# Optimization experiments

Hardware: AMD Instinct MI355X
Metric: run time of the kernel (lower is better)

The kernel has to match this reference:

```python
import jax, jax.numpy as jnp
import numpy as np

D_MODEL = 768
NHEAD = 12
HEAD_DIM = D_MODEL // NHEAD


def setup_inputs() -> dict:
    key = jax.random.key(0)
    ks = jax.random.split(key, 9)
    B, S = 1, 4096
    scale = 1.0 / np.sqrt(D_MODEL)
    x = jax.random.normal(ks[0], (B, S, D_MODEL), dtype=jnp.float32)
    # Linear params: weight [out,in] torch convention, bias [out]
    wq = jax.random.normal(ks[1], (D_MODEL, D_MODEL), dtype=jnp.float32) * scale
    bq = jnp.zeros((D_MODEL,), dtype=jnp.float32)
    wk = jax.random.normal(ks[2], (D_MODEL, D_MODEL), dtype=jnp.float32) * scale
    bk = jnp.zeros((D_MODEL,), dtype=jnp.float32)
    wv = jax.random.normal(ks[3], (D_MODEL, D_MODEL), dtype=jnp.float32) * scale
    bv = jnp.zeros((D_MODEL,), dtype=jnp.float32)
    wo = jax.random.normal(ks[4], (D_MODEL, D_MODEL), dtype=jnp.float32) * scale
    bo = jnp.zeros((D_MODEL,), dtype=jnp.float32)
    return {"x": x, "wq": wq, "bq": bq, "wk": wk, "bk": bk,
            "wv": wv, "bv": bv, "wo": wo, "bo": bo}


def reference(x, wq, bq, wk, bk, wv, bv, wo, bo):
    B, S, D = x.shape
    H, Hd = NHEAD, HEAD_DIM
    # projections (torch Linear: x @ W^T + b)
    q = (x @ wq.T + bq).reshape(B, S, H, Hd).transpose(0, 2, 1, 3)  # [B,H,S,Hd]
    k = (x @ wk.T + bk).reshape(B, S, H, Hd).transpose(0, 2, 1, 3)
    v = (x @ wv.T + bv).reshape(B, S, H, Hd).transpose(0, 2, 1, 3)
    scores = jnp.einsum('bhsd,bhtd->bhst', q, k) / jnp.sqrt(jnp.float32(Hd))  # [B,H,S,S]
    probs = jax.nn.softmax(scores, axis=-1)
    attn = jnp.einsum('bhst,bhtd->bhsd', probs, v)  # [B,H,S,Hd]
    attn = attn.transpose(0, 2, 1, 3).reshape(B, S, D)
    return attn @ wo.T + bo
```

## Files before the change

kernel.cpp:

```cpp
#include <hip/hip_runtime.h>
#include <hip/hip_bf16.h>

typedef __attribute__((ext_vector_type(8))) __bf16 bf16x8;
typedef __attribute__((ext_vector_type(4))) __bf16 bf16x4;
typedef __attribute__((ext_vector_type(4))) float f32x4;
typedef __attribute__((ext_vector_type(16))) float f32x16;
typedef __attribute__((ext_vector_type(2))) unsigned u32x2;

#define D_MODEL 768
#define SEQ     4096
#define NH      12
#define HD      64

#define QSCALE (0.125f * 1.44269504088896f)

__device__ __forceinline__ void gload_lds16(const void* g, void* l) {
    __builtin_amdgcn_global_load_lds(
        (const __attribute__((address_space(1))) void*)g,
        (__attribute__((address_space(3))) void*)l, 16, 0, 0);
}

__device__ __forceinline__ u32x2 plswap(unsigned a, unsigned b) {
    return __builtin_amdgcn_permlane32_swap(a, b, false, false);
}

__global__ __launch_bounds__(256) void cvt_kernel(
    const float* __restrict__ x,  const float* __restrict__ wq,
    const float* __restrict__ wk, const float* __restrict__ wv,
    const float* __restrict__ wo,
    __bf16* __restrict__ xb,  __bf16* __restrict__ wqb,
    __bf16* __restrict__ wkb, __bf16* __restrict__ wvb,
    __bf16* __restrict__ wob)
{
    const int XV = SEQ * D_MODEL / 4;
    const int WV = D_MODEL * D_MODEL / 4;
    const int total = XV + 4 * WV;
    for (int i = blockIdx.x * blockDim.x + threadIdx.x; i < total;
         i += gridDim.x * blockDim.x) {
        const float* src; __bf16* dst; int j;
        if      (i < XV)          { src = x;  dst = xb;  j = i; }
        else if (i < XV + WV)     { src = wq; dst = wqb; j = i - XV; }
        else if (i < XV + 2*WV)   { src = wk; dst = wkb; j = i - XV - WV; }
        else if (i < XV + 3*WV)   { src = wv; dst = wvb; j = i - XV - 2*WV; }
        else                      { src = wo; dst = wob; j = i - XV - 3*WV; }
        float4 v = ((const float4*)src)[j];
        bf16x4 o;
        o[0] = (__bf16)v.x; o[1] = (__bf16)v.y;
        o[2] = (__bf16)v.z; o[3] = (__bf16)v.w;
        ((bf16x4*)dst)[j] = o;
    }
}

__device__ __forceinline__ void gemm128_core(
    const __bf16* __restrict__ A, const __bf16* __restrict__ B, int KD,
    f32x4 acc[4][4], __bf16 (*As)[64], __bf16 (*Bs)[64])
{
    const int t = threadIdx.x;
    const int lane = t & 63, wid = t >> 6;
    const int wm = (wid & 1) * 64, wn = (wid >> 1) * 64;
    const int lr = lane & 15, lc = lane >> 4;
    const int rl = lane >> 3;
    const int cs = (lane & 7) ^ rl;

    const __bf16* ag = A + (size_t)(wid * 32 + rl) * KD + cs * 8;
    const __bf16* bg = B + (size_t)(wid * 32 + rl) * KD + cs * 8;

    for (int kt = 0; kt < KD / 64; ++kt) {
        __syncthreads();
        #pragma unroll
        for (int i = 0; i < 4; ++i) {
            gload_lds16(ag + (size_t)i * 8 * KD + kt * 64,
                        &As[wid * 32 + i * 8][0]);
            gload_lds16(bg + (size_t)i * 8 * KD + kt * 64,
                        &Bs[wid * 32 + i * 8][0]);
        }
        __syncthreads();

        #pragma unroll
        for (int kh = 0; kh < 2; ++kh) {
            bf16x8 af[4], bfr[4];
            #pragma unroll
            for (int mi = 0; mi < 4; ++mi)
                af[mi] = *(const bf16x8*)
                    &As[wm + mi * 16 + lr][(((kh << 2) | lc) ^ (lr & 7)) * 8];
            #pragma unroll
            for (int ni = 0; ni < 4; ++ni)
                bfr[ni] = *(const bf16x8*)
                    &Bs[wn + ni * 16 + lr][(((kh << 2) | lc) ^ (lr & 7)) * 8];
            __builtin_amdgcn_s_setprio(1);
            #pragma unroll
            for (int mi = 0; mi < 4; ++mi)
                #pragma unroll
                for (int ni = 0; ni < 4; ++ni)
                    acc[mi][ni] = __builtin_amdgcn_mfma_f32_16x16x32_bf16(
                        af[mi], bfr[ni], acc[mi][ni], 0, 0, 0);
            __builtin_amdgcn_s_setprio(0);
        }
    }
}

__global__ __launch_bounds__(256) void qkv_gemm(
    const __bf16* __restrict__ xb,
    const __bf16* __restrict__ wqb, const __bf16* __restrict__ wkb,
    const __bf16* __restrict__ wvb,
    const float* __restrict__ bq, const float* __restrict__ bk,
    const float* __restrict__ bv,
    __bf16* __restrict__ Qo, __bf16* __restrict__ Ko,
    __bf16* __restrict__ Vto)
{
    __shared__ __bf16 As[128][64];
    __shared__ __bf16 Bs[128][64];
    const int bm = blockIdx.x;
    const int seg = blockIdx.y / 6, bn = blockIdx.y % 6;
    const __bf16* B  = (seg == 0) ? wqb : (seg == 1) ? wkb : wvb;
    const float* bias = (seg == 0) ? bq : (seg == 1) ? bk : bv;

    f32x4 acc[4][4] = {};
    gemm128_core(xb + (size_t)bm * 128 * D_MODEL,
                 B  + (size_t)bn * 128 * D_MODEL, D_MODEL, acc, As, Bs);

    const int t = threadIdx.x, lane = t & 63, wid = t >> 6;
    const int wm = (wid & 1) * 64, wn = (wid >> 1) * 64;
    const int lr = lane & 15, lc = lane >> 4;
    const int m0 = bm * 128 + wm, n0 = bn * 128 + wn;

    if (seg < 2) {
        __bf16* O = (seg == 0) ? Qo : Ko;
        const float sc = (seg == 0) ? QSCALE : 1.0f;
        #pragma unroll
        for (int mi = 0; mi < 4; ++mi)
            #pragma unroll
            for (int ni = 0; ni < 4; ++ni) {
                int col = n0 + ni * 16 + lr;
                float bb = bias[col];
                #pragma unroll
                for (int r = 0; r < 4; ++r)
                    O[(size_t)(m0 + mi * 16 + lc * 4 + r) * D_MODEL + col] =
                        (__bf16)((acc[mi][ni][r] + bb) * sc);
            }
    } else {
        #pragma unroll
        for (int mi = 0; mi < 4; ++mi)
            #pragma unroll
            for (int ni = 0; ni < 4; ++ni) {
                int col = n0 + ni * 16 + lr;
                float bb = bias[col];
                bf16x4 pk;
                #pragma unroll
                for (int r = 0; r < 4; ++r)
                    pk[r] = (__bf16)(acc[mi][ni][r] + bb);
                *(bf16x4*)&Vto[(size_t)col * SEQ + m0 + mi * 16 + lc * 4] = pk;
            }
    }
}

__global__ __launch_bounds__(256) void attn_kernel(
    const __bf16* __restrict__ Q, const __bf16* __restrict__ K,
    const __bf16* __restrict__ Vt, __bf16* __restrict__ Attn)
{
    __shared__ __align__(16) char LDSc[49152];
    __bf16 (*Ks)[32][64] = (__bf16(*)[32][64])(LDSc);
    __bf16 (*Vs)[64][32] = (__bf16(*)[64][32])(LDSc + 24576);
    float* Mg = (float*)LDSc;
    float* Ml = (float*)(LDSc + 24576);

    const int bid = blockIdx.x;
    const int swz = (bid & 7) * 96 + (bid >> 3);
    const int h  = swz >> 6;
    const int q0 = (swz & 63) * 64;

    const int t = threadIdx.x, lane = t & 63, wid = t >> 6;
    const int qs = wid & 1, half = wid >> 1;
    const int ql = lane & 31, hi = lane >> 5;
    const int s7 = ql & 7;
    const int v2s = (ql >> 1) & 3;

    const int krl = lane >> 3, kcs = (lane & 7) ^ (lane >> 3);
    const int vrl = lane >> 2, vcs = (lane & 3) ^ ((lane >> 3) & 3);
    const __bf16* kg = K +
        (size_t)(half * 2048 + qs * 16 + krl) * D_MODEL + h * HD + kcs * 8;
    const __bf16* vg = Vt +
        (size_t)(h * HD + qs * 32 + vrl) * SEQ + half * 2048 + vcs * 8;

    const __bf16* qrow = Q + (size_t)(q0 + qs * 32 + ql) * D_MODEL + h * HD;
    bf16x8 qf[4];
    #pragma unroll
    for (int k4 = 0; k4 < 4; ++k4)
        qf[k4] = *(const bf16x8*)&qrow[k4 * 16 + hi * 8];

    f32x16 acc0 = {}, acc1 = {};
    f32x16 lacc = {};

    #define STAGE(BUF, TT) do {                                               \
        const __bf16* kgt = kg + (size_t)(TT) * 32 * D_MODEL;                 \
        const __bf16* vgt = vg + (TT) * 32;                                   \
        gload_lds16(kgt,                    &Ks[half*3 + (BUF)][qs*16][0]);   \
        gload_lds16(kgt + 8 * D_MODEL,      &Ks[half*3 + (BUF)][qs*16+8][0]); \
        gload_lds16(vgt,                    &Vs[half*3 + (BUF)][qs*32][0]);   \
        gload_lds16(vgt + (size_t)16 * SEQ, &Vs[half*3 + (BUF)][qs*32+16][0]);\
    } while (0)

    STAGE(0, 0);

    const int NT = 2048 / 32;

#define ATILE(CUR, NXT, PT, DOPF) do {                                        \
    if (DOPF) {                                                               \
        STAGE(NXT, PT);                                                       \
        asm volatile("s_waitcnt vmcnt(4)" ::: "memory");                      \
    } else {                                                                  \
        asm volatile("s_waitcnt vmcnt(0)" ::: "memory");                      \
    }                                                                         \
    __builtin_amdgcn_s_barrier();                                             \
    f32x16 st = {};                                                           \
    __builtin_amdgcn_s_setprio(1);                                            \
    _Pragma("unroll")                                                         \
    for (int k4 = 0; k4 < 4; ++k4) {                                          \
        bf16x8 kf = *(const bf16x8*)                                          \
            &Ks[half*3 + (CUR)][ql][((k4*2 + hi) ^ s7) * 8];                  \
        st = __builtin_amdgcn_mfma_f32_32x32x16_bf16(kf, qf[k4], st, 0,0,0);  \
    }                                                                         \
    __builtin_amdgcn_s_setprio(0);                                            \
                 \
    _Pragma("unroll")                                                         \
    for (int r = 0; r < 16; ++r) st[r] = exp2f(st[r]);                        \
    lacc += st;                                                               \
                                               \
    unsigned wA[4], wB[4];                                                    \
    _Pragma("unroll")                                                         \
    for (int g = 0; g < 4; ++g) {                                             \
        union { __bf16 h2[2]; unsigned u; } pa, pb;                           \
        pa.h2[0] = (__bf16)st[4*g + 0]; pa.h2[1] = (__bf16)st[4*g + 1];       \
        pb.h2[0] = (__bf16)st[4*g + 2]; pb.h2[1] = (__bf16)st[4*g + 3];       \
        wA[g] = pa.u; wB[g] = pb.u;                                           \
    }                                                                         \
    __builtin_amdgcn_s_setprio(1);                                            \
    _Pragma("unroll")                                                         \
    for (int kb = 0; kb < 2; ++kb) {                                          \
        u32x2 sA = plswap(wA[2*kb], wA[2*kb + 1]);                            \
        u32x2 sB = plswap(wB[2*kb], wB[2*kb + 1]);                            \
        union { unsigned u[4]; bf16x8 v; } fb;                                \
        fb.u[0] = sA[0]; fb.u[1] = sB[0]; fb.u[2] = sA[1]; fb.u[3] = sB[1];   \
        bf16x8 vf0 = *(const bf16x8*)                                         \
            &Vs[half*3 + (CUR)][ql][((kb*2 + hi) ^ v2s) * 8];                 \
        bf16x8 vf1 = *(const bf16x8*)                                         \
            &Vs[half*3 + (CUR)][32 + ql][((kb*2 + hi) ^ v2s) * 8];            \
        acc0 = __builtin_amdgcn_mfma_f32_32x32x16_bf16(vf0, fb.v, acc0,0,0,0);\
        acc1 = __builtin_amdgcn_mfma_f32_32x32x16_bf16(vf1, fb.v, acc1,0,0,0);\
    }                                                                         \
    __builtin_amdgcn_s_setprio(0);                                            \
} while (0)

    for (int kk = 0; kk < 63; kk += 3) {
        ATILE(0, 1, kk + 1, 1);
        ATILE(1, 2, kk + 2, 1);
        ATILE(2, 0, kk + 3, (kk + 3 < NT));
    }
    ATILE(0, 1, 0, 0);
#undef ATILE
#undef STAGE

    float l_r;
    {
        float t8[8];
        #pragma unroll
        for (int i = 0; i < 8; ++i) t8[i] = lacc[i] + lacc[i + 8];
        #pragma unroll
        for (int i = 0; i < 4; ++i) t8[i] += t8[i + 4];
        l_r = (t8[0] + t8[1]) + (t8[2] + t8[3]);
        u32x2 rp = plswap(__float_as_uint(l_r), __float_as_uint(l_r));
        l_r = __uint_as_float(rp[0]) + __uint_as_float(rp[1]);
    }

    __syncthreads();
    if (half == 1) {
        float* mybuf = Mg + qs * 2048 + lane * 32;
        #pragma unroll
        for (int j = 0; j < 4; ++j) {
            f32x4 v; v[0]=acc0[4*j]; v[1]=acc0[4*j+1]; v[2]=acc0[4*j+2]; v[3]=acc0[4*j+3];
            *(f32x4*)&mybuf[(j ^ s7) * 4] = v;
        }
        #pragma unroll
        for (int j = 0; j < 4; ++j) {
            f32x4 v; v[0]=acc1[4*j]; v[1]=acc1[4*j+1]; v[2]=acc1[4*j+2]; v[3]=acc1[4*j+3];
            *(f32x4*)&mybuf[((4 + j) ^ s7) * 4] = v;
        }
        Ml[qs * 64 + lane] = l_r;
    }
    __syncthreads();
    if (half == 0) {
        float l1 = Ml[qs * 64 + lane];
        float li = 1.0f / (l_r + l1);
        const float* obuf = Mg + qs * 2048 + lane * 32;

        __bf16* orow = Attn + (size_t)(q0 + qs * 32 + ql) * D_MODEL
                       + h * HD + hi * 4;
        #pragma unroll
        for (int g = 0; g < 4; ++g) {
            f32x4 a1 = *(const f32x4*)&obuf[(g ^ s7) * 4];
            union { __bf16 h4[4]; uint2 v2; } w;
            #pragma unroll
            for (int i = 0; i < 4; ++i)
                w.h4[i] = (__bf16)((acc0[4*g+i] + a1[i]) * li);
            *(uint2*)&orow[g * 8] = w.v2;

            f32x4 b1 = *(const f32x4*)&obuf[((4 + g) ^ s7) * 4];
            #pragma unroll
            for (int i = 0; i < 4; ++i)
                w.h4[i] = (__bf16)((acc1[4*g+i] + b1[i]) * li);
            *(uint2*)&orow[32 + g * 8] = w.v2;
        }
    }
}

__global__ __launch_bounds__(256) void out_gemm(
    const __bf16* __restrict__ Ab, const __bf16* __restrict__ wob,
    const float* __restrict__ bo, float* __restrict__ out)
{
    __shared__ __bf16 As[128][64];
    __shared__ __bf16 Bs[128][64];
    const int bm = blockIdx.x, bn = blockIdx.y;
    f32x4 acc[4][4] = {};
    gemm128_core(Ab  + (size_t)bm * 128 * D_MODEL,
                 wob + (size_t)bn * 128 * D_MODEL, D_MODEL, acc, As, Bs);

    const int t = threadIdx.x, lane = t & 63, wid = t >> 6;
    const int wm = (wid & 1) * 64, wn = (wid >> 1) * 64;
    const int lr = lane & 15, lc = lane >> 4;
    const int m0 = bm * 128 + wm, n0 = bn * 128 + wn;
    #pragma unroll
    for (int mi = 0; mi < 4; ++mi)
        #pragma unroll
        for (int ni = 0; ni < 4; ++ni) {
            int col = n0 + ni * 16 + lr;
            float bb = bo[col];
            #pragma unroll
            for (int r = 0; r < 4; ++r)
                out[(size_t)(m0 + mi * 16 + lc * 4 + r) * D_MODEL + col] =
                    acc[mi][ni][r] + bb;
        }
}

extern "C" void kernel_launch(void* const* d_in, const int* in_sizes, int n_in,
                              void* d_out, int out_size, void* d_ws, size_t ws_size,
                              hipStream_t stream) {
    const float* x  = (const float*)d_in[0];
    const float* wq = (const float*)d_in[1];
    const float* bq = (const float*)d_in[2];
    const float* wk = (const float*)d_in[3];
    const float* bk = (const float*)d_in[4];
    const float* wv = (const float*)d_in[5];
    const float* bv = (const float*)d_in[6];
    const float* wo = (const float*)d_in[7];
    const float* bo = (const float*)d_in[8];

    char* ws = (char*)d_ws;
    const size_t XB_SZ = (size_t)SEQ * D_MODEL * 2;
    const size_t W_SZ  = (size_t)D_MODEL * D_MODEL * 2;
    __bf16* xb  = (__bf16*)(ws);
    __bf16* wqb = (__bf16*)(ws + XB_SZ);
    __bf16* wkb = (__bf16*)(ws + XB_SZ + W_SZ);
    __bf16* wvb = (__bf16*)(ws + XB_SZ + 2 * W_SZ);
    __bf16* wob = (__bf16*)(ws + XB_SZ + 3 * W_SZ);
    __bf16* Qb  = (__bf16*)(ws + XB_SZ + 4 * W_SZ);
    __bf16* Kb  = (__bf16*)(ws + 2 * XB_SZ + 4 * W_SZ);
    __bf16* Vtb = (__bf16*)(ws + 3 * XB_SZ + 4 * W_SZ);
    __bf16* Ab  = (__bf16*)(ws + 4 * XB_SZ + 4 * W_SZ);

    cvt_kernel<<<1024, 256, 0, stream>>>(x, wq, wk, wv, wo,
                                         xb, wqb, wkb, wvb, wob);
    qkv_gemm<<<dim3(32, 18), 256, 0, stream>>>(xb, wqb, wkb, wvb,
                                               bq, bk, bv, Qb, Kb, Vtb);
    attn_kernel<<<768, 256, 0, stream>>>(Qb, Kb, Vtb, Ab);
    out_gemm<<<dim3(32, 6), 256, 0, stream>>>(Ab, wob, bo, (float*)d_out);
}
```

Measured before the change: 151.0 us.

## Double-buffer GEMM LDS tiles and swizzle block order for XCD locality

The shared GEMM core now ping-pongs between two LDS buffers: each iteration issues the next k-tile's global-to-LDS loads before computing on the current one, with explicit vmcnt waits and barriers in place of the old load-then-sync loop. Both GEMM kernels move to a 1D grid whose block index is remapped so that consecutive blocks on the same XCD work on neighbouring tiles, which should improve L2 reuse. The goal is to hide global load latency behind MFMA work. The cost is double the LDS per block, which can lower occupancy, and the pipeline relies on hand-written waitcnt counts that assume K is a multiple of 128 (KD is 768 here, so NK = 12 is even).

```diff
diff --git a/kernel.cpp b/kernel.cpp
--- a/kernel.cpp
+++ b/kernel.cpp
@@ -53,7 +53,7 @@
 
 __device__ __forceinline__ void gemm128_core(
     const __bf16* __restrict__ A, const __bf16* __restrict__ B, int KD,
-    f32x4 acc[4][4], __bf16 (*As)[64], __bf16 (*Bs)[64])
+    f32x4 acc[4][4], __bf16 (*As)[128][64], __bf16 (*Bs)[128][64])
 {
     const int t = threadIdx.x;
     const int lane = t & 63, wid = t >> 6;
@@ -65,38 +65,59 @@
     const __bf16* ag = A + (size_t)(wid * 32 + rl) * KD + cs * 8;
     const __bf16* bg = B + (size_t)(wid * 32 + rl) * KD + cs * 8;
 
-    for (int kt = 0; kt < KD / 64; ++kt) {
-        __syncthreads();
-        #pragma unroll
-        for (int i = 0; i < 4; ++i) {
-            gload_lds16(ag + (size_t)i * 8 * KD + kt * 64,
-                        &As[wid * 32 + i * 8][0]);
-            gload_lds16(bg + (size_t)i * 8 * KD + kt * 64,
-                        &Bs[wid * 32 + i * 8][0]);
+#define GSTAGE(BUF, KT) do {                                                  \
+        _Pragma("unroll")                                                     \
+        for (int i = 0; i < 4; ++i) {                                         \
+            gload_lds16(ag + (size_t)i * 8 * KD + (KT) * 64,                  \
+                        &As[BUF][wid * 32 + i * 8][0]);                       \
+            gload_lds16(bg + (size_t)i * 8 * KD + (KT) * 64,                  \
+                        &Bs[BUF][wid * 32 + i * 8][0]);                       \
+        }                                                                     \
+    } while (0)
+
+#define GCOMP(BUF) do {                                                       \
+        _Pragma("unroll")                                                     \
+        for (int kh = 0; kh < 2; ++kh) {                                      \
+            bf16x8 af[4], bfr[4];                                             \
+            _Pragma("unroll")                                                 \
+            for (int mi = 0; mi < 4; ++mi)                                    \
+                af[mi] = *(const bf16x8*)                                     \
+                    &As[BUF][wm + mi*16 + lr][(((kh<<2)|lc) ^ (lr&7)) * 8];   \
+            _Pragma("unroll")                                                 \
+            for (int ni = 0; ni < 4; ++ni)                                    \
+                bfr[ni] = *(const bf16x8*)                                    \
+                    &Bs[BUF][wn + ni*16 + lr][(((kh<<2)|lc) ^ (lr&7)) * 8];   \
+            __builtin_amdgcn_s_setprio(1);                                    \
+            _Pragma("unroll")                                                 \
+            for (int mi = 0; mi < 4; ++mi)                                    \
+                _Pragma("unroll")                                             \
+                for (int ni = 0; ni < 4; ++ni)                                \
+                    acc[mi][ni] = __builtin_amdgcn_mfma_f32_16x16x32_bf16(    \
+                        af[mi], bfr[ni], acc[mi][ni], 0, 0, 0);               \
+            __builtin_amdgcn_s_setprio(0);                                    \
+        }                                                                     \
+    } while (0)
+
+    GSTAGE(0, 0);
+    const int NK = KD / 64;
+    for (int kt = 0; kt < NK; kt += 2) {
+        __builtin_amdgcn_s_barrier();
+        GSTAGE(1, kt + 1);
+        asm volatile("s_waitcnt vmcnt(8)" ::: "memory");
+        __builtin_amdgcn_s_barrier();
+        GCOMP(0);
+        __builtin_amdgcn_s_barrier();
+        if (kt + 2 < NK) {
+            GSTAGE(0, kt + 2);
+            asm volatile("s_waitcnt vmcnt(8)" ::: "memory");
+        } else {
+            asm volatile("s_waitcnt vmcnt(0)" ::: "memory");
         }
-        __syncthreads();
-
-        #pragma unroll
-        for (int kh = 0; kh < 2; ++kh) {
-            bf16x8 af[4], bfr[4];
-            #pragma unroll
-            for (int mi = 0; mi < 4; ++mi)
-                af[mi] = *(const bf16x8*)
-                    &As[wm + mi * 16 + lr][(((kh << 2) | lc) ^ (lr & 7)) * 8];
-            #pragma unroll
-            for (int ni = 0; ni < 4; ++ni)
-                bfr[ni] = *(const bf16x8*)
-                    &Bs[wn + ni * 16 + lr][(((kh << 2) | lc) ^ (lr & 7)) * 8];
-            __builtin_amdgcn_s_setprio(1);
-            #pragma unroll
-            for (int mi = 0; mi < 4; ++mi)
-                #pragma unroll
-                for (int ni = 0; ni < 4; ++ni)
-                    acc[mi][ni] = __builtin_amdgcn_mfma_f32_16x16x32_bf16(
-                        af[mi], bfr[ni], acc[mi][ni], 0, 0, 0);
-            __builtin_amdgcn_s_setprio(0);
-        }
-    }
+        __builtin_amdgcn_s_barrier();
+        GCOMP(1);
+    }
+#undef GSTAGE
+#undef GCOMP
 }
 
 __global__ __launch_bounds__(256) void qkv_gemm(
@@ -108,10 +129,13 @@
     __bf16* __restrict__ Qo, __bf16* __restrict__ Ko,
     __bf16* __restrict__ Vto)
 {
-    __shared__ __bf16 As[128][64];
-    __shared__ __bf16 Bs[128][64];
-    const int bm = blockIdx.x;
-    const int seg = blockIdx.y / 6, bn = blockIdx.y % 6;
+    __shared__ __bf16 As[2][128][64];
+    __shared__ __bf16 Bs[2][128][64];
+    const int b = blockIdx.x;
+    const int swz = (b & 7) * 72 + (b >> 3);
+    const int bm = swz & 31;
+    const int yy = swz >> 5;
+    const int seg = yy / 6, bn = yy % 6;
     const __bf16* B  = (seg == 0) ? wqb : (seg == 1) ? wkb : wvb;
     const float* bias = (seg == 0) ? bq : (seg == 1) ? bk : bv;
 
@@ -317,9 +341,11 @@
     const __bf16* __restrict__ Ab, const __bf16* __restrict__ wob,
     const float* __restrict__ bo, float* __restrict__ out)
 {
-    __shared__ __bf16 As[128][64];
-    __shared__ __bf16 Bs[128][64];
-    const int bm = blockIdx.x, bn = blockIdx.y;
+    __shared__ __bf16 As[2][128][64];
+    __shared__ __bf16 Bs[2][128][64];
+    const int b = blockIdx.x;
+    const int swz = (b & 7) * 24 + (b >> 3);
+    const int bm = swz & 31, bn = swz >> 5;
     f32x4 acc[4][4] = {};
     gemm128_core(Ab  + (size_t)bm * 128 * D_MODEL,
                  wob + (size_t)bn * 128 * D_MODEL, D_MODEL, acc, As, Bs);
@@ -369,8 +395,8 @@
 
     cvt_kernel<<<1024, 256, 0, stream>>>(x, wq, wk, wv, wo,
                                          xb, wqb, wkb, wvb, wob);
-    qkv_gemm<<<dim3(32, 18), 256, 0, stream>>>(xb, wqb, wkb, wvb,
-                                               bq, bk, bv, Qb, Kb, Vtb);
+    qkv_gemm<<<576, 256, 0, stream>>>(xb, wqb, wkb, wvb,
+                                      bq, bk, bv, Qb, Kb, Vtb);
     attn_kernel<<<768, 256, 0, stream>>>(Qb, Kb, Vtb, Ab);
-    out_gemm<<<dim3(32, 6), 256, 0, stream>>>(Ab, wob, bo, (float*)d_out);
-}
+    out_gemm<<<192, 256, 0, stream>>>(Ab, wob, bo, (float*)d_out);
+}
```

After: 151.0 us (median of 3 runs). No clear change (-0.0%).

## Fuse fp32-to-bf16 conversion into GEMM tile loads and remove conversion kernel

Applied to the files above, without the earlier changes.

The separate conversion kernel is removed. Both GEMMs now load fp32 inputs and weights through registers, convert them to bf16 while writing into swizzled LDS, and prefetch the next K tile in registers before the MMA phase. Block indices are also remapped with an XCD-style swizzle. This saves one kernel launch and one full pass that wrote and reread the bf16 copies. In exchange, every GEMM block re-reads fp32 data, so the weights are converted redundantly, and the direct global-to-LDS loads are replaced by register-staged stores.

```diff
diff --git a/kernel.cpp b/kernel.cpp
--- a/kernel.cpp
+++ b/kernel.cpp
@@ -24,85 +24,19 @@
     return __builtin_amdgcn_permlane32_swap(a, b, false, false);
 }
 
-__global__ __launch_bounds__(256) void cvt_kernel(
-    const float* __restrict__ x,  const float* __restrict__ wq,
-    const float* __restrict__ wk, const float* __restrict__ wv,
-    const float* __restrict__ wo,
-    __bf16* __restrict__ xb,  __bf16* __restrict__ wqb,
-    __bf16* __restrict__ wkb, __bf16* __restrict__ wvb,
-    __bf16* __restrict__ wob)
-{
-    const int XV = SEQ * D_MODEL / 4;
-    const int WV = D_MODEL * D_MODEL / 4;
-    const int total = XV + 4 * WV;
-    for (int i = blockIdx.x * blockDim.x + threadIdx.x; i < total;
-         i += gridDim.x * blockDim.x) {
-        const float* src; __bf16* dst; int j;
-        if      (i < XV)          { src = x;  dst = xb;  j = i; }
-        else if (i < XV + WV)     { src = wq; dst = wqb; j = i - XV; }
-        else if (i < XV + 2*WV)   { src = wk; dst = wkb; j = i - XV - WV; }
-        else if (i < XV + 3*WV)   { src = wv; dst = wvb; j = i - XV - 2*WV; }
-        else                      { src = wo; dst = wob; j = i - XV - 3*WV; }
-        float4 v = ((const float4*)src)[j];
-        bf16x4 o;
-        o[0] = (__bf16)v.x; o[1] = (__bf16)v.y;
-        o[2] = (__bf16)v.z; o[3] = (__bf16)v.w;
-        ((bf16x4*)dst)[j] = o;
-    }
-}
-
-__device__ __forceinline__ void gemm128_core(
-    const __bf16* __restrict__ A, const __bf16* __restrict__ B, int KD,
-    f32x4 acc[4][4], __bf16 (*As)[64], __bf16 (*Bs)[64])
-{
-    const int t = threadIdx.x;
-    const int lane = t & 63, wid = t >> 6;
-    const int wm = (wid & 1) * 64, wn = (wid >> 1) * 64;
-    const int lr = lane & 15, lc = lane >> 4;
-    const int rl = lane >> 3;
-    const int cs = (lane & 7) ^ rl;
-
-    const __bf16* ag = A + (size_t)(wid * 32 + rl) * KD + cs * 8;
-    const __bf16* bg = B + (size_t)(wid * 32 + rl) * KD + cs * 8;
-
-    for (int kt = 0; kt < KD / 64; ++kt) {
-        __syncthreads();
-        #pragma unroll
-        for (int i = 0; i < 4; ++i) {
-            gload_lds16(ag + (size_t)i * 8 * KD + kt * 64,
-                        &As[wid * 32 + i * 8][0]);
-            gload_lds16(bg + (size_t)i * 8 * KD + kt * 64,
-                        &Bs[wid * 32 + i * 8][0]);
-        }
-        __syncthreads();
-
-        #pragma unroll
-        for (int kh = 0; kh < 2; ++kh) {
-            bf16x8 af[4], bfr[4];
-            #pragma unroll
-            for (int mi = 0; mi < 4; ++mi)
-                af[mi] = *(const bf16x8*)
-                    &As[wm + mi * 16 + lr][(((kh << 2) | lc) ^ (lr & 7)) * 8];
-            #pragma unroll
-            for (int ni = 0; ni < 4; ++ni)
-                bfr[ni] = *(const bf16x8*)
-                    &Bs[wn + ni * 16 + lr][(((kh << 2) | lc) ^ (lr & 7)) * 8];
-            __builtin_amdgcn_s_setprio(1);
-            #pragma unroll
-            for (int mi = 0; mi < 4; ++mi)
-                #pragma unroll
-                for (int ni = 0; ni < 4; ++ni)
-                    acc[mi][ni] = __builtin_amdgcn_mfma_f32_16x16x32_bf16(
-                        af[mi], bfr[ni], acc[mi][ni], 0, 0, 0);
-            __builtin_amdgcn_s_setprio(0);
-        }
-    }
+__device__ __forceinline__ bf16x8 cvt8(const float4& a, const float4& b) {
+    union { __bf16 h8[8]; bf16x8 v; } p;
+    p.h8[0] = (__bf16)a.x; p.h8[1] = (__bf16)a.y;
+    p.h8[2] = (__bf16)a.z; p.h8[3] = (__bf16)a.w;
+    p.h8[4] = (__bf16)b.x; p.h8[5] = (__bf16)b.y;
+    p.h8[6] = (__bf16)b.z; p.h8[7] = (__bf16)b.w;
+    return p.v;
 }
 
 __global__ __launch_bounds__(256) void qkv_gemm(
-    const __bf16* __restrict__ xb,
-    const __bf16* __restrict__ wqb, const __bf16* __restrict__ wkb,
-    const __bf16* __restrict__ wvb,
+    const float* __restrict__ x,
+    const float* __restrict__ wq, const float* __restrict__ wk,
+    const float* __restrict__ wv,
     const float* __restrict__ bq, const float* __restrict__ bk,
     const float* __restrict__ bv,
     __bf16* __restrict__ Qo, __bf16* __restrict__ Ko,
@@ -110,20 +44,74 @@
 {
     __shared__ __bf16 As[128][64];
     __shared__ __bf16 Bs[128][64];
-    const int bm = blockIdx.x;
-    const int seg = blockIdx.y / 6, bn = blockIdx.y % 6;
-    const __bf16* B  = (seg == 0) ? wqb : (seg == 1) ? wkb : wvb;
+    const int b = blockIdx.x;
+    const int swz = (b & 7) * 72 + (b >> 3);
+    const int bm = swz & 31;
+    const int yy = swz >> 5;
+    const int seg = yy / 6, bn = yy % 6;
+    const float* W   = (seg == 0) ? wq : (seg == 1) ? wk : wv;
     const float* bias = (seg == 0) ? bq : (seg == 1) ? bk : bv;
-
-    f32x4 acc[4][4] = {};
-    gemm128_core(xb + (size_t)bm * 128 * D_MODEL,
-                 B  + (size_t)bn * 128 * D_MODEL, D_MODEL, acc, As, Bs);
 
     const int t = threadIdx.x, lane = t & 63, wid = t >> 6;
     const int wm = (wid & 1) * 64, wn = (wid >> 1) * 64;
     const int lr = lane & 15, lc = lane >> 4;
+    const int r = t >> 1;
+    const int hb = (t & 1) * 4;
+
+    const float* ax = x + (size_t)(bm * 128 + r) * D_MODEL + hb * 8;
+    const float* bx = W + (size_t)(bn * 128 + r) * D_MODEL + hb * 8;
+
+    f32x4 acc[4][4] = {};
+
+    float4 av[8], bv8[8];
+    #pragma unroll
+    for (int j = 0; j < 8; ++j) {
+        av[j]  = *(const float4*)(ax + j * 4);
+        bv8[j] = *(const float4*)(bx + j * 4);
+    }
+
+    const int NK = D_MODEL / 64;
+    for (int kt = 0; kt < NK; ++kt) {
+        __syncthreads();
+        #pragma unroll
+        for (int i = 0; i < 4; ++i) {
+            *(bf16x8*)&As[r][((hb + i) ^ (r & 7)) * 8] =
+                cvt8(av[2 * i], av[2 * i + 1]);
+            *(bf16x8*)&Bs[r][((hb + i) ^ (r & 7)) * 8] =
+                cvt8(bv8[2 * i], bv8[2 * i + 1]);
+        }
+        if (kt + 1 < NK) {
+            #pragma unroll
+            for (int j = 0; j < 8; ++j) {
+                av[j]  = *(const float4*)(ax + (kt + 1) * 64 + j * 4);
+                bv8[j] = *(const float4*)(bx + (kt + 1) * 64 + j * 4);
+            }
+        }
+        __syncthreads();
+
+        #pragma unroll
+        for (int kh = 0; kh < 2; ++kh) {
+            bf16x8 af[4], bfr[4];
+            #pragma unroll
+            for (int mi = 0; mi < 4; ++mi)
+                af[mi] = *(const bf16x8*)
+                    &As[wm + mi * 16 + lr][(((kh << 2) | lc) ^ (lr & 7)) * 8];
+            #pragma unroll
+            for (int ni = 0; ni < 4; ++ni)
+                bfr[ni] = *(const bf16x8*)
+                    &Bs[wn + ni * 16 + lr][(((kh << 2) | lc) ^ (lr & 7)) * 8];
+            __builtin_amdgcn_s_setprio(1);
+            #pragma unroll
+            for (int mi = 0; mi < 4; ++mi)
+                #pragma unroll
+                for (int ni = 0; ni < 4; ++ni)
+                    acc[mi][ni] = __builtin_amdgcn_mfma_f32_16x16x32_bf16(
+                        af[mi], bfr[ni], acc[mi][ni], 0, 0, 0);
+            __builtin_amdgcn_s_setprio(0);
+        }
+    }
+
     const int m0 = bm * 128 + wm, n0 = bn * 128 + wn;
-
     if (seg < 2) {
         __bf16* O = (seg == 0) ? Qo : Ko;
         const float sc = (seg == 0) ? QSCALE : 1.0f;
@@ -134,9 +122,9 @@
                 int col = n0 + ni * 16 + lr;
                 float bb = bias[col];
                 #pragma unroll
-                for (int r = 0; r < 4; ++r)
-                    O[(size_t)(m0 + mi * 16 + lc * 4 + r) * D_MODEL + col] =
-                        (__bf16)((acc[mi][ni][r] + bb) * sc);
+                for (int rr = 0; rr < 4; ++rr)
+                    O[(size_t)(m0 + mi * 16 + lc * 4 + rr) * D_MODEL + col] =
+                        (__bf16)((acc[mi][ni][rr] + bb) * sc);
             }
     } else {
         #pragma unroll
@@ -147,8 +135,8 @@
                 float bb = bias[col];
                 bf16x4 pk;
                 #pragma unroll
-                for (int r = 0; r < 4; ++r)
-                    pk[r] = (__bf16)(acc[mi][ni][r] + bb);
+                for (int rr = 0; rr < 4; ++rr)
+                    pk[rr] = (__bf16)(acc[mi][ni][rr] + bb);
                 *(bf16x4*)&Vto[(size_t)col * SEQ + m0 + mi * 16 + lc * 4] = pk;
             }
     }
@@ -314,19 +302,74 @@
 }
 
 __global__ __launch_bounds__(256) void out_gemm(
-    const __bf16* __restrict__ Ab, const __bf16* __restrict__ wob,
+    const __bf16* __restrict__ Ab, const float* __restrict__ wo,
     const float* __restrict__ bo, float* __restrict__ out)
 {
     __shared__ __bf16 As[128][64];
     __shared__ __bf16 Bs[128][64];
-    const int bm = blockIdx.x, bn = blockIdx.y;
-    f32x4 acc[4][4] = {};
-    gemm128_core(Ab  + (size_t)bm * 128 * D_MODEL,
-                 wob + (size_t)bn * 128 * D_MODEL, D_MODEL, acc, As, Bs);
+    const int b = blockIdx.x;
+    const int swz = (b & 7) * 24 + (b >> 3);
+    const int bm = swz & 31, bn = swz >> 5;
 
     const int t = threadIdx.x, lane = t & 63, wid = t >> 6;
     const int wm = (wid & 1) * 64, wn = (wid >> 1) * 64;
     const int lr = lane & 15, lc = lane >> 4;
+    const int r = t >> 1;
+    const int hb = (t & 1) * 4;
+
+    const __bf16* ax = Ab + (size_t)(bm * 128 + r) * D_MODEL + hb * 8;
+    const float*  bx = wo + (size_t)(bn * 128 + r) * D_MODEL + hb * 8;
+
+    f32x4 acc[4][4] = {};
+
+    bf16x8 av[4];
+    float4 bv8[8];
+    #pragma unroll
+    for (int j = 0; j < 4; ++j) av[j] = *(const bf16x8*)(ax + j * 8);
+    #pragma unroll
+    for (int j = 0; j < 8; ++j) bv8[j] = *(const float4*)(bx + j * 4);
+
+    const int NK = D_MODEL / 64;
+    for (int kt = 0; kt < NK; ++kt) {
+        __syncthreads();
+        #pragma unroll
+        for (int i = 0; i < 4; ++i) {
+            *(bf16x8*)&As[r][((hb + i) ^ (r & 7)) * 8] = av[i];
+            *(bf16x8*)&Bs[r][((hb + i) ^ (r & 7)) * 8] =
+                cvt8(bv8[2 * i], bv8[2 * i + 1]);
+        }
+        if (kt + 1 < NK) {
+            #pragma unroll
+            for (int j = 0; j < 4; ++j)
+                av[j] = *(const bf16x8*)(ax + (kt + 1) * 64 + j * 8);
+            #pragma unroll
+            for (int j = 0; j < 8; ++j)
+                bv8[j] = *(const float4*)(bx + (kt + 1) * 64 + j * 4);
+        }
+        __syncthreads();
+
+        #pragma unroll
+        for (int kh = 0; kh < 2; ++kh) {
+            bf16x8 af[4], bfr[4];
+            #pragma unroll
+            for (int mi = 0; mi < 4; ++mi)
+                af[mi] = *(const bf16x8*)
+                    &As[wm + mi * 16 + lr][(((kh << 2) | lc) ^ (lr & 7)) * 8];
+            #pragma unroll
+            for (int ni = 0; ni < 4; ++ni)
+                bfr[ni] = *(const bf16x8*)
+                    &Bs[wn + ni * 16 + lr][(((kh << 2) | lc) ^ (lr & 7)) * 8];
+            __builtin_amdgcn_s_setprio(1);
+            #pragma unroll
+            for (int mi = 0; mi < 4; ++mi)
+                #pragma unroll
+                for (int ni = 0; ni < 4; ++ni)
+                    acc[mi][ni] = __builtin_amdgcn_mfma_f32_16x16x32_bf16(
+                        af[mi], bfr[ni], acc[mi][ni], 0, 0, 0);
+            __builtin_amdgcn_s_setprio(0);
+        }
+    }
+
     const int m0 = bm * 128 + wm, n0 = bn * 128 + wn;
     #pragma unroll
     for (int mi = 0; mi < 4; ++mi)
@@ -335,9 +378,9 @@
             int col = n0 + ni * 16 + lr;
             float bb = bo[col];
             #pragma unroll
-            for (int r = 0; r < 4; ++r)
-                out[(size_t)(m0 + mi * 16 + lc * 4 + r) * D_MODEL + col] =
-                    acc[mi][ni][r] + bb;
+            for (int rr = 0; rr < 4; ++rr)
+                out[(size_t)(m0 + mi * 16 + lc * 4 + rr) * D_MODEL + col] =
+                    acc[mi][ni][rr] + bb;
         }
 }
 
@@ -356,21 +399,13 @@
 
     char* ws = (char*)d_ws;
     const size_t XB_SZ = (size_t)SEQ * D_MODEL * 2;
-    const size_t W_SZ  = (size_t)D_MODEL * D_MODEL * 2;
-    __bf16* xb  = (__bf16*)(ws);
-    __bf16* wqb = (__bf16*)(ws + XB_SZ);
-    __bf16* wkb = (__bf16*)(ws + XB_SZ + W_SZ);
-    __bf16* wvb = (__bf16*)(ws + XB_SZ + 2 * W_SZ);
-    __bf16* wob = (__bf16*)(ws + XB_SZ + 3 * W_SZ);
-    __bf16* Qb  = (__bf16*)(ws + XB_SZ + 4 * W_SZ);
-    __bf16* Kb  = (__bf16*)(ws + 2 * XB_SZ + 4 * W_SZ);
-    __bf16* Vtb = (__bf16*)(ws + 3 * XB_SZ + 4 * W_SZ);
-    __bf16* Ab  = (__bf16*)(ws + 4 * XB_SZ + 4 * W_SZ);
-
-    cvt_kernel<<<1024, 256, 0, stream>>>(x, wq, wk, wv, wo,
-                                         xb, wqb, wkb, wvb, wob);
-    qkv_gemm<<<dim3(32, 18), 256, 0, stream>>>(xb, wqb, wkb, wvb,
-                                               bq, bk, bv, Qb, Kb, Vtb);
+    __bf16* Qb  = (__bf16*)(ws);
+    __bf16* Kb  = (__bf16*)(ws + XB_SZ);
+    __bf16* Vtb = (__bf16*)(ws + 2 * XB_SZ);
+    __bf16* Ab  = (__bf16*)(ws + 3 * XB_SZ);
+
+    qkv_gemm<<<576, 256, 0, stream>>>(x, wq, wk, wv,
+                                      bq, bk, bv, Qb, Kb, Vtb);
     attn_kernel<<<768, 256, 0, stream>>>(Qb, Kb, Vtb, Ab);
-    out_gemm<<<dim3(32, 6), 256, 0, stream>>>(Ab, wob, bo, (float*)d_out);
-}
+    out_gemm<<<192, 256, 0, stream>>>(Ab, wo, bo, (float*)d_out);
+}
```

After: 213.5 us. 1.41x slower.
